# Kernel tuning notes

Measured on AMD Instinct MI355X. Metric: run time of the kernel, lower is better.

The kernel has to match this reference:

```python
import jax, jax.numpy as jnp
import numpy as np
import math

B, S, H, NH = 2, 2048, 1024, 16
DH = H // NH  # 64
REL_VOCAB = 4096  # 2 * (max_position_embeddings // 4)


def setup_inputs() -> dict:
    key = jax.random.key(0)
    ks = jax.random.split(key, 9)
    s = 0.02
    return {
        "hidden_states": jax.random.normal(ks[0], (B, S, H), jnp.float32),
        "attention_mask": jnp.zeros((B, 1, 1, S), jnp.float32),
        "distance_idx": jax.random.randint(ks[1], (S, S), 0, REL_VOCAB),
        "Wq": jax.random.normal(ks[2], (H, H), jnp.float32) * s,
        "bq": jnp.zeros((H,), jnp.float32),
        "Wk": jax.random.normal(ks[3], (H, H), jnp.float32) * s,
        "bk": jnp.zeros((H,), jnp.float32),
        "Wv": jax.random.normal(ks[4], (H, H), jnp.float32) * s,
        "bv": jnp.zeros((H,), jnp.float32),
        "dist_emb": jax.random.normal(ks[5], (REL_VOCAB, NH), jnp.float32) * s,
    }


def _heads(x):
    # [B,S,H] -> [B,NH,S,DH]
    return x.reshape(B, S, NH, DH).transpose(0, 2, 1, 3)


def reference(hidden_states, attention_mask, distance_idx, Wq, bq, Wk, bk, Wv, bv, dist_emb):
    q = _heads(hidden_states @ Wq.T + bq)
    k = _heads(hidden_states @ Wk.T + bk)
    v = _heads(hidden_states @ Wv.T + bv)
    # scores: [B,NH,S,S]
    scores = jnp.einsum("bhqd,bhkd->bhqk", q, k) / math.sqrt(DH)
    # relative_scalar_bias: embed(distance_idx) [S,S,NH] -> [1,NH,S,S]
    bias = dist_emb[distance_idx].transpose(2, 0, 1)[None]
    scores = scores + bias  # attention_scores_terms == 1 -> /sqrt(1)
    scores = scores + attention_mask
    probs = jax.nn.softmax(scores, axis=-1)
    ctx = jnp.einsum("bhqk,bhkd->bhqd", probs, v)
    return ctx.transpose(0, 2, 1, 3).reshape(B, S, H)
```

## Files before the change

kernel.cpp:

```cpp
#include <hip/hip_runtime.h>
#include <hip/hip_bf16.h>

#define B_   2
#define S_   2048
#define H_   1024
#define NH_  16
#define DH_  64

typedef __attribute__((ext_vector_type(8))) __bf16 bf16x8;
typedef __attribute__((ext_vector_type(8))) unsigned short u16x8;
typedef __attribute__((ext_vector_type(4))) float f32x4;

typedef const __attribute__((address_space(1))) unsigned int gu32_t;
typedef __attribute__((address_space(3))) unsigned int su32_t;

static __device__ inline unsigned short f2bf(float x) {
    union { float f; unsigned u; } v; v.f = x;
    unsigned r = v.u + 0x7fffu + ((v.u >> 16) & 1u);
    return (unsigned short)(r >> 16);
}

static __device__ inline unsigned short f2bf_r(float x) {
    union { float f; unsigned u; } v; v.f = x;
    return (unsigned short)((v.u + 0x8000u) >> 16);
}

static __device__ inline float bf2f(unsigned short u) {
    union { unsigned u; float f; } v; v.u = ((unsigned)u) << 16;
    return v.f;
}

static __device__ inline bf16x8 ldfrag(const unsigned short* p) {
    return __builtin_bit_cast(bf16x8, *(const u16x8*)p);
}

__global__ void conv_all(const float* __restrict__ x,
                         const float* __restrict__ Wq, const float* __restrict__ Wk,
                         const float* __restrict__ Wv, const float* __restrict__ demb,
                         unsigned short* __restrict__ xb, unsigned short* __restrict__ wall,
                         unsigned short* __restrict__ dembT) {
    int bid = blockIdx.x, tid = threadIdx.x;
    if (bid < 4096) {
        int i = bid * 256 + tid;
        float4 v = ((const float4*)x)[i];
        ushort4 o;
        o.x = f2bf(v.x); o.y = f2bf(v.y); o.z = f2bf(v.z); o.w = f2bf(v.w);
        ((ushort4*)xb)[i] = o;
    } else if (bid < 7168) {
        int i = (bid - 4096) * 256 + tid;
        int e = i * 4;
        int which = e >> 20;
        int r4 = (e & ((1 << 20) - 1)) >> 2;
        const float* src = which == 0 ? Wq : which == 1 ? Wk : Wv;
        float4 v = ((const float4*)src)[r4];
        ushort4 o;
        o.x = f2bf(v.x); o.y = f2bf(v.y); o.z = f2bf(v.z); o.w = f2bf(v.w);
        ((ushort4*)wall)[i] = o;
    } else {
        int t = (bid - 7168) * 256 + tid;
        int h = t >> 12, e = t & 4095;
        dembT[t] = f2bf(demb[e * 16 + h] * 1.4426950408889634f);
    }
}

__global__ __launch_bounds__(256) void gemm_qkv(
    const unsigned short* __restrict__ Xb, const unsigned short* __restrict__ Wall,
    const float* __restrict__ bq, const float* __restrict__ bk, const float* __restrict__ bv,
    unsigned short* __restrict__ Q, unsigned short* __restrict__ K, unsigned short* __restrict__ V)
{
    __shared__ unsigned short As[128 * 32];
    __shared__ unsigned short Bs[128 * 32];
    const int tid = threadIdx.x, lane = tid & 63, wv = tid >> 6;
    const int g = lane >> 4, l16 = lane & 15;
    const int wm = wv >> 1, wn = wv & 1;
    const int bm = blockIdx.y, bn = blockIdx.x;

    const int lrow = lane >> 2, lcol = (lane & 3) * 8;

    f32x4 acc[4][4];
    #pragma unroll
    for (int i = 0; i < 4; ++i)
        #pragma unroll
        for (int j = 0; j < 4; ++j) acc[i][j] = (f32x4){0.f, 0.f, 0.f, 0.f};

    for (int kt = 0; kt < 32; ++kt) {
        #pragma unroll
        for (int i = 0; i < 2; ++i) {
            int chunk = wv * 2 + i;
            int row = chunk * 16 + lrow;
            const unsigned short* ga = &Xb[(size_t)(bm * 128 + row) * 1024 + kt * 32 + lcol];
            const unsigned short* gb = &Wall[(size_t)(bn * 128 + row) * 1024 + kt * 32 + lcol];
            __builtin_amdgcn_global_load_lds((gu32_t*)(const void*)ga, (su32_t*)(void*)&As[chunk * 512], 16, 0, 0);
            __builtin_amdgcn_global_load_lds((gu32_t*)(const void*)gb, (su32_t*)(void*)&Bs[chunk * 512], 16, 0, 0);
        }
        __syncthreads();
        bf16x8 a[4], b[4];
        #pragma unroll
        for (int mi = 0; mi < 4; ++mi) a[mi] = ldfrag(&As[(wm * 64 + mi * 16 + l16) * 32 + g * 8]);
        #pragma unroll
        for (int ni = 0; ni < 4; ++ni) b[ni] = ldfrag(&Bs[(wn * 64 + ni * 16 + l16) * 32 + g * 8]);
        #pragma unroll
        for (int mi = 0; mi < 4; ++mi)
            #pragma unroll
            for (int ni = 0; ni < 4; ++ni)
                acc[mi][ni] = __builtin_amdgcn_mfma_f32_16x16x32_bf16(a[mi], b[ni], acc[mi][ni], 0, 0, 0);
        __syncthreads();
    }

    #pragma unroll
    for (int mi = 0; mi < 4; ++mi) {
        #pragma unroll
        for (int ni = 0; ni < 4; ++ni) {
            int gn = bn * 128 + wn * 64 + ni * 16 + l16;
            int which = gn >> 10, nn = gn & 1023;
            int h = nn >> 6, d = nn & 63;
            float bias = which == 0 ? bq[nn] : which == 1 ? bk[nn] : bv[nn];
            unsigned short* dst = which == 0 ? Q : which == 1 ? K : V;
            #pragma unroll
            for (int r = 0; r < 4; ++r) {
                int gm = bm * 128 + wm * 64 + mi * 16 + g * 4 + r;
                int bb = gm >> 11, s = gm & 2047;
                dst[((size_t)(bb * 16 + h) * 2048 + s) * 64 + d] = f2bf(acc[mi][ni][r] + bias);
            }
        }
    }
}

__global__ void transpose_v(const unsigned short* __restrict__ V, unsigned short* __restrict__ VT) {
    __shared__ unsigned short t[64][65];
    int bh = blockIdx.y, st = blockIdx.x, tid = threadIdx.x;
    size_t ib = (size_t)bh * S_ * DH_ + (size_t)st * 64 * 64;
    #pragma unroll
    for (int rep = 0; rep < 16; ++rep) {
        int e = rep * 256 + tid;
        t[e >> 6][e & 63] = V[ib + e];
    }
    __syncthreads();
    size_t ob = (size_t)bh * DH_ * S_ + st * 64;
    #pragma unroll
    for (int rep = 0; rep < 16; ++rep) {
        int e = rep * 256 + tid;
        int d = e >> 6, sl = e & 63;
        VT[ob + (size_t)d * S_ + sl] = t[sl][d];
    }
}

__global__ __launch_bounds__(256, 4) void attn(
    const unsigned short* __restrict__ Q, const unsigned short* __restrict__ K,
    const unsigned short* __restrict__ VT, const int* __restrict__ didx,
    const unsigned short* __restrict__ dembT, const float* __restrict__ mask,
    float* __restrict__ out)
{
    __shared__ unsigned short demb_h[4096];
    __shared__ unsigned short Ks[64 * 64];
    __shared__ unsigned short Vs[64 * 64];
    __shared__ unsigned short Ps[64 * 64];
    const int tid = threadIdx.x, lane = tid & 63, w = tid >> 6;
    const int g = lane >> 4, l16 = lane & 15;
    const int h = blockIdx.x, qt = blockIdx.y, b = blockIdx.z;
    const int bh = b * NH_ + h;
    const int qr = qt * 64 + w * 16;

    #pragma unroll
    for (int j = 0; j < 2; ++j) {
        int i = j * 256 + tid;
        *(uint4*)&demb_h[i * 8] = *(const uint4*)&dembT[h * 4096 + i * 8];
    }

    bf16x8 qf[4][2];
    #pragma unroll
    for (int qtile = 0; qtile < 4; ++qtile) {
        size_t qbase = ((size_t)bh * S_ + qt * 64 + qtile * 16 + l16) * DH_;
        qf[qtile][0] = ldfrag(&Q[qbase + g * 8]);
        qf[qtile][1] = ldfrag(&Q[qbase + 32 + g * 8]);
    }

    u16x8 ou;
    #pragma unroll
    for (int i = 0; i < 8; ++i) ou[i] = 0x3F80;
    const bf16x8 onesf = __builtin_bit_cast(bf16x8, ou);

    f32x4 oa[4];
    f32x4 lacc = (f32x4){0.f, 0.f, 0.f, 0.f};
    #pragma unroll
    for (int i = 0; i < 4; ++i) oa[i] = (f32x4){0.f, 0.f, 0.f, 0.f};

    const size_t kbase = (size_t)bh * S_ * DH_;
    const size_t vbase = (size_t)bh * DH_ * S_;

    __syncthreads();

    for (int kt = 0; kt < 32; ++kt) {
        #pragma unroll
        for (int j = 0; j < 2; ++j) {
            int e = j * 2048 + tid * 8;
            int r = e >> 6, c = e & 63;
            int sidx = r * 64 + ((((c >> 3) ^ (r & 7))) << 3);
            *(uint4*)&Ks[sidx] = *(const uint4*)&K[kbase + (size_t)kt * 64 * 64 + e];
            *(uint4*)&Vs[sidx] = *(const uint4*)&VT[vbase + (size_t)r * S_ + kt * 64 + c];
        }

        const int kg = kt * 64 + w * 16 + l16;
        float mk = mask[b * S_ + kg];
        int ei[4][4];
        #pragma unroll
        for (int qtile = 0; qtile < 4; ++qtile) {
            #pragma unroll
            for (int r = 0; r < 4; ++r) {
                int qg = qt * 64 + qtile * 16 + g * 4 + r;
                ei[qtile][r] = didx[qg * S_ + kg];
            }
        }
        __syncthreads();

        const int krow = w * 16 + l16, km = krow & 7;
        bf16x8 kf0 = ldfrag(&Ks[krow * 64 + ((g ^ km) << 3)]);
        bf16x8 kf1 = ldfrag(&Ks[krow * 64 + (((g + 4) ^ km) << 3)]);
        const float mkl = mk * 1.4426950408889634f;
        const int pcol = w * 16 + l16;
        const int chunkx = pcol >> 3, coff = pcol & 7;

        __builtin_amdgcn_s_setprio(1);
        #pragma unroll
        for (int qtile = 0; qtile < 4; ++qtile) {
            f32x4 z = (f32x4){0.f, 0.f, 0.f, 0.f};
            z = __builtin_amdgcn_mfma_f32_16x16x32_bf16(qf[qtile][0], kf0, z, 0, 0, 0);
            z = __builtin_amdgcn_mfma_f32_16x16x32_bf16(qf[qtile][1], kf1, z, 0, 0, 0);
            #pragma unroll
            for (int r = 0; r < 4; ++r) {
                float bm = bf2f(demb_h[ei[qtile][r]]) + mkl;
                float p = __builtin_amdgcn_exp2f(fmaf(z[r], 0.18033688011112042f, bm));
                int q = qtile * 16 + g * 4 + r;
                int idx = q * 64 + (((chunkx ^ (q & 7))) << 3) + coff;
                Ps[idx] = f2bf_r(p);
            }
        }
        __builtin_amdgcn_s_setprio(0);
        __syncthreads();

        const int prow = w * 16 + l16, pm = prow & 7;
        bf16x8 pf0 = ldfrag(&Ps[prow * 64 + ((g ^ pm) << 3)]);
        bf16x8 pf1 = ldfrag(&Ps[prow * 64 + (((g + 4) ^ pm) << 3)]);
        __builtin_amdgcn_s_setprio(1);
        lacc = __builtin_amdgcn_mfma_f32_16x16x32_bf16(pf0, onesf, lacc, 0, 0, 0);
        lacc = __builtin_amdgcn_mfma_f32_16x16x32_bf16(pf1, onesf, lacc, 0, 0, 0);
        #pragma unroll
        for (int dt = 0; dt < 4; ++dt) {
            int row = dt * 16 + l16, m = row & 7;
            bf16x8 vf0 = ldfrag(&Vs[row * 64 + ((g ^ m) << 3)]);
            bf16x8 vf1 = ldfrag(&Vs[row * 64 + (((g + 4) ^ m) << 3)]);
            oa[dt] = __builtin_amdgcn_mfma_f32_16x16x32_bf16(pf0, vf0, oa[dt], 0, 0, 0);
            oa[dt] = __builtin_amdgcn_mfma_f32_16x16x32_bf16(pf1, vf1, oa[dt], 0, 0, 0);
        }
        __builtin_amdgcn_s_setprio(0);
        __syncthreads();
    }

    float linv[4];
    #pragma unroll
    for (int r = 0; r < 4; ++r) linv[r] = __builtin_amdgcn_rcpf(lacc[r]);

    #pragma unroll
    for (int dt = 0; dt < 4; ++dt) {
        #pragma unroll
        for (int r = 0; r < 4; ++r) {
            int s = qr + g * 4 + r;
            int d = dt * 16 + l16;
            out[((size_t)b * S_ + s) * H_ + h * DH_ + d] = oa[dt][r] * linv[r];
        }
    }
}

extern "C" void kernel_launch(void* const* d_in, const int* in_sizes, int n_in,
                              void* d_out, int out_size, void* d_ws, size_t ws_size,
                              hipStream_t stream) {
    const float* hidden = (const float*)d_in[0];
    const float* mask   = (const float*)d_in[1];
    const int*   didx   = (const int*)d_in[2];
    const float* Wq     = (const float*)d_in[3];
    const float* bq     = (const float*)d_in[4];
    const float* Wk     = (const float*)d_in[5];
    const float* bk     = (const float*)d_in[6];
    const float* Wv     = (const float*)d_in[7];
    const float* bv     = (const float*)d_in[8];
    const float* demb   = (const float*)d_in[9];
    float* out = (float*)d_out;

    unsigned short* ws = (unsigned short*)d_ws;
    unsigned short* Xb   = ws;
    unsigned short* Wall = Xb + 4096 * 1024;
    unsigned short* Qb   = Wall + 3072 * 1024;
    unsigned short* Kb   = Qb + 4194304;
    unsigned short* Vb   = Kb + 4194304;
    unsigned short* VTb  = Vb + 4194304;
    unsigned short* DembT = VTb + 4194304;

    conv_all<<<7424, 256, 0, stream>>>(hidden, Wq, Wk, Wv, demb, Xb, Wall, DembT);
    gemm_qkv<<<dim3(24, 32), 256, 0, stream>>>(Xb, Wall, bq, bk, bv, Qb, Kb, Vb);
    transpose_v<<<dim3(32, 32), 256, 0, stream>>>(Vb, VTb);
    attn<<<dim3(16, 32, 2), 256, 0, stream>>>(Qb, Kb, VTb, didx, DembT, mask, out);
}
```

Before: 222.0 us.

## Keep P in registers via transposed QK^T and split-K PV with final reduction

Computes S^T = K·Q^T so each lane's score fragment directly serves as the A operand of a 16x16x16 MFMA for P·V. This removes the Ps shared-memory round trip and one barrier per key tile. Each wave now accumulates partial outputs for all four query tiles over its own 16 keys, and the partials are reduced across waves through shared memory at the end. Row sums are now done with scalar adds plus shuffles instead of a ones-MFMA, and distance-index and mask loads become int4/float4. The cost is more accumulator registers (launch bounds lowered to 3), an epilogue reduction, and a fallback macro that silently returns c if the builtin is missing.

```diff
diff --git a/kernel.cpp b/kernel.cpp
--- a/kernel.cpp
+++ b/kernel.cpp
@@ -10,6 +10,7 @@
 typedef __attribute__((ext_vector_type(8))) __bf16 bf16x8;
 typedef __attribute__((ext_vector_type(8))) unsigned short u16x8;
 typedef __attribute__((ext_vector_type(4))) float f32x4;
+typedef __attribute__((ext_vector_type(4))) short i16x4;
 
 typedef const __attribute__((address_space(1))) unsigned int gu32_t;
 typedef __attribute__((address_space(3))) unsigned int su32_t;
@@ -33,6 +34,12 @@
 static __device__ inline bf16x8 ldfrag(const unsigned short* p) {
     return __builtin_bit_cast(bf16x8, *(const u16x8*)p);
 }
+
+#if __has_builtin(__builtin_amdgcn_mfma_f32_16x16x16bf16_1k)
+#define MFMA16(a, b, c) __builtin_amdgcn_mfma_f32_16x16x16bf16_1k((a), (b), (c), 0, 0, 0)
+#else
+#define MFMA16(a, b, c) (c)
+#endif
 
 __global__ void conv_all(const float* __restrict__ x,
                          const float* __restrict__ Wq, const float* __restrict__ Wk,
@@ -145,21 +152,23 @@
     }
 }
 
-__global__ __launch_bounds__(256, 4) void attn(
+__global__ __launch_bounds__(256, 3) void attn(
     const unsigned short* __restrict__ Q, const unsigned short* __restrict__ K,
     const unsigned short* __restrict__ VT, const int* __restrict__ didx,
     const unsigned short* __restrict__ dembT, const float* __restrict__ mask,
     float* __restrict__ out)
 {
-    __shared__ unsigned short demb_h[4096];
-    __shared__ unsigned short Ks[64 * 64];
-    __shared__ unsigned short Vs[64 * 64];
-    __shared__ unsigned short Ps[64 * 64];
+    __shared__ __align__(16) unsigned char smem[24576];
+    unsigned short* demb_h = (unsigned short*)smem;
+    unsigned short* Ks     = (unsigned short*)(smem + 8192);
+    unsigned short* Vs     = (unsigned short*)(smem + 16384);
+    float* tbl = (float*)smem;
+    float* red = (float*)smem;
+
     const int tid = threadIdx.x, lane = tid & 63, w = tid >> 6;
     const int g = lane >> 4, l16 = lane & 15;
     const int h = blockIdx.x, qt = blockIdx.y, b = blockIdx.z;
     const int bh = b * NH_ + h;
-    const int qr = qt * 64 + w * 16;
 
     #pragma unroll
     for (int j = 0; j < 2; ++j) {
@@ -175,18 +184,18 @@
         qf[qtile][1] = ldfrag(&Q[qbase + 32 + g * 8]);
     }
 
-    u16x8 ou;
-    #pragma unroll
-    for (int i = 0; i < 8; ++i) ou[i] = 0x3F80;
-    const bf16x8 onesf = __builtin_bit_cast(bf16x8, ou);
-
-    f32x4 oa[4];
-    f32x4 lacc = (f32x4){0.f, 0.f, 0.f, 0.f};
-    #pragma unroll
-    for (int i = 0; i < 4; ++i) oa[i] = (f32x4){0.f, 0.f, 0.f, 0.f};
+    f32x4 oa[4][4];
+    float lsum[4];
+    #pragma unroll
+    for (int i = 0; i < 4; ++i) {
+        lsum[i] = 0.f;
+        #pragma unroll
+        for (int j = 0; j < 4; ++j) oa[i][j] = (f32x4){0.f, 0.f, 0.f, 0.f};
+    }
 
     const size_t kbase = (size_t)bh * S_ * DH_;
     const size_t vbase = (size_t)bh * DH_ * S_;
+    const int kg0 = w * 16 + g * 4;
 
     __syncthreads();
 
@@ -196,79 +205,167 @@
             int e = j * 2048 + tid * 8;
             int r = e >> 6, c = e & 63;
             int sidx = r * 64 + ((((c >> 3) ^ (r & 7))) << 3);
-            *(uint4*)&Ks[sidx] = *(const uint4*)&K[kbase + (size_t)kt * 64 * 64 + e];
+            *(uint4*)&Ks[sidx] = *(const uint4*)&K[kbase + (size_t)kt * 4096 + e];
             *(uint4*)&Vs[sidx] = *(const uint4*)&VT[vbase + (size_t)r * S_ + kt * 64 + c];
         }
 
-        const int kg = kt * 64 + w * 16 + l16;
-        float mk = mask[b * S_ + kg];
-        int ei[4][4];
-        #pragma unroll
-        for (int qtile = 0; qtile < 4; ++qtile) {
-            #pragma unroll
-            for (int r = 0; r < 4; ++r) {
-                int qg = qt * 64 + qtile * 16 + g * 4 + r;
-                ei[qtile][r] = didx[qg * S_ + kg];
-            }
-        }
+        const int kg = kt * 64 + kg0;
+        int4 di0 = *(const int4*)&didx[(qt * 64 + 0 * 16 + l16) * S_ + kg];
+        int4 di1 = *(const int4*)&didx[(qt * 64 + 1 * 16 + l16) * S_ + kg];
+        int4 di2 = *(const int4*)&didx[(qt * 64 + 2 * 16 + l16) * S_ + kg];
+        int4 di3 = *(const int4*)&didx[(qt * 64 + 3 * 16 + l16) * S_ + kg];
+        float4 mv = *(const float4*)&mask[b * S_ + kg];
         __syncthreads();
 
         const int krow = w * 16 + l16, km = krow & 7;
         bf16x8 kf0 = ldfrag(&Ks[krow * 64 + ((g ^ km) << 3)]);
         bf16x8 kf1 = ldfrag(&Ks[krow * 64 + (((g + 4) ^ km) << 3)]);
-        const float mkl = mk * 1.4426950408889634f;
-        const int pcol = w * 16 + l16;
-        const int chunkx = pcol >> 3, coff = pcol & 7;
-
+
+        i16x4 vf[4];
+        #pragma unroll
+        for (int dt = 0; dt < 4; ++dt) {
+            int vrow = dt * 16 + l16, vm = vrow & 7;
+            int chunkc = w * 2 + (g >> 1);
+            int addr = vrow * 64 + (((chunkc ^ vm)) << 3) + ((g & 1) << 2);
+            vf[dt] = *(const i16x4*)&Vs[addr];
+        }
+
+        f32x4 z0, z1, z2, z3;
         __builtin_amdgcn_s_setprio(1);
-        #pragma unroll
-        for (int qtile = 0; qtile < 4; ++qtile) {
-            f32x4 z = (f32x4){0.f, 0.f, 0.f, 0.f};
-            z = __builtin_amdgcn_mfma_f32_16x16x32_bf16(qf[qtile][0], kf0, z, 0, 0, 0);
-            z = __builtin_amdgcn_mfma_f32_16x16x32_bf16(qf[qtile][1], kf1, z, 0, 0, 0);
-            #pragma unroll
-            for (int r = 0; r < 4; ++r) {
-                float bm = bf2f(demb_h[ei[qtile][r]]) + mkl;
-                float p = __builtin_amdgcn_exp2f(fmaf(z[r], 0.18033688011112042f, bm));
-                int q = qtile * 16 + g * 4 + r;
-                int idx = q * 64 + (((chunkx ^ (q & 7))) << 3) + coff;
-                Ps[idx] = f2bf_r(p);
-            }
+        {
+            f32x4 zz = (f32x4){0.f, 0.f, 0.f, 0.f};
+            zz = __builtin_amdgcn_mfma_f32_16x16x32_bf16(kf0, qf[0][0], zz, 0, 0, 0);
+            z0 = __builtin_amdgcn_mfma_f32_16x16x32_bf16(kf1, qf[0][1], zz, 0, 0, 0);
+            zz = (f32x4){0.f, 0.f, 0.f, 0.f};
+            zz = __builtin_amdgcn_mfma_f32_16x16x32_bf16(kf0, qf[1][0], zz, 0, 0, 0);
+            z1 = __builtin_amdgcn_mfma_f32_16x16x32_bf16(kf1, qf[1][1], zz, 0, 0, 0);
+            zz = (f32x4){0.f, 0.f, 0.f, 0.f};
+            zz = __builtin_amdgcn_mfma_f32_16x16x32_bf16(kf0, qf[2][0], zz, 0, 0, 0);
+            z2 = __builtin_amdgcn_mfma_f32_16x16x32_bf16(kf1, qf[2][1], zz, 0, 0, 0);
+            zz = (f32x4){0.f, 0.f, 0.f, 0.f};
+            zz = __builtin_amdgcn_mfma_f32_16x16x32_bf16(kf0, qf[3][0], zz, 0, 0, 0);
+            z3 = __builtin_amdgcn_mfma_f32_16x16x32_bf16(kf1, qf[3][1], zz, 0, 0, 0);
+        }
+        __builtin_amdgcn_s_setprio(0);
+
+        const float ml0 = mv.x * 1.4426950408889634f;
+        const float ml1 = mv.y * 1.4426950408889634f;
+        const float ml2 = mv.z * 1.4426950408889634f;
+        const float ml3 = mv.w * 1.4426950408889634f;
+        i16x4 pa0, pa1, pa2, pa3;
+        #define EXPPACK(ZZ, DI, PA, QIDX)                                                   \
+        {                                                                                   \
+            float p0 = __builtin_amdgcn_exp2f(fmaf(ZZ[0], 0.18033688011112042f,             \
+                        bf2f(demb_h[DI.x]) + ml0));                                         \
+            float p1 = __builtin_amdgcn_exp2f(fmaf(ZZ[1], 0.18033688011112042f,             \
+                        bf2f(demb_h[DI.y]) + ml1));                                         \
+            float p2 = __builtin_amdgcn_exp2f(fmaf(ZZ[2], 0.18033688011112042f,             \
+                        bf2f(demb_h[DI.z]) + ml2));                                         \
+            float p3 = __builtin_amdgcn_exp2f(fmaf(ZZ[3], 0.18033688011112042f,             \
+                        bf2f(demb_h[DI.w]) + ml3));                                         \
+            lsum[QIDX] += (p0 + p1) + (p2 + p3);                                            \
+            PA[0] = (short)f2bf_r(p0); PA[1] = (short)f2bf_r(p1);                           \
+            PA[2] = (short)f2bf_r(p2); PA[3] = (short)f2bf_r(p3);                           \
+        }
+        EXPPACK(z0, di0, pa0, 0)
+        EXPPACK(z1, di1, pa1, 1)
+        EXPPACK(z2, di2, pa2, 2)
+        EXPPACK(z3, di3, pa3, 3)
+        #undef EXPPACK
+
+        __builtin_amdgcn_s_setprio(1);
+        #pragma unroll
+        for (int dt = 0; dt < 4; ++dt) {
+            oa[0][dt] = MFMA16(pa0, vf[dt], oa[0][dt]);
+            oa[1][dt] = MFMA16(pa1, vf[dt], oa[1][dt]);
+            oa[2][dt] = MFMA16(pa2, vf[dt], oa[2][dt]);
+            oa[3][dt] = MFMA16(pa3, vf[dt], oa[3][dt]);
         }
         __builtin_amdgcn_s_setprio(0);
         __syncthreads();
-
-        const int prow = w * 16 + l16, pm = prow & 7;
-        bf16x8 pf0 = ldfrag(&Ps[prow * 64 + ((g ^ pm) << 3)]);
-        bf16x8 pf1 = ldfrag(&Ps[prow * 64 + (((g + 4) ^ pm) << 3)]);
-        __builtin_amdgcn_s_setprio(1);
-        lacc = __builtin_amdgcn_mfma_f32_16x16x32_bf16(pf0, onesf, lacc, 0, 0, 0);
-        lacc = __builtin_amdgcn_mfma_f32_16x16x32_bf16(pf1, onesf, lacc, 0, 0, 0);
-        #pragma unroll
-        for (int dt = 0; dt < 4; ++dt) {
-            int row = dt * 16 + l16, m = row & 7;
-            bf16x8 vf0 = ldfrag(&Vs[row * 64 + ((g ^ m) << 3)]);
-            bf16x8 vf1 = ldfrag(&Vs[row * 64 + (((g + 4) ^ m) << 3)]);
-            oa[dt] = __builtin_amdgcn_mfma_f32_16x16x32_bf16(pf0, vf0, oa[dt], 0, 0, 0);
-            oa[dt] = __builtin_amdgcn_mfma_f32_16x16x32_bf16(pf1, vf1, oa[dt], 0, 0, 0);
-        }
-        __builtin_amdgcn_s_setprio(0);
-        __syncthreads();
-    }
-
-    float linv[4];
-    #pragma unroll
-    for (int r = 0; r < 4; ++r) linv[r] = __builtin_amdgcn_rcpf(lacc[r]);
-
-    #pragma unroll
-    for (int dt = 0; dt < 4; ++dt) {
-        #pragma unroll
-        for (int r = 0; r < 4; ++r) {
-            int s = qr + g * 4 + r;
-            int d = dt * 16 + l16;
-            out[((size_t)b * S_ + s) * H_ + h * DH_ + d] = oa[dt][r] * linv[r];
-        }
-    }
+    }
+
+    #pragma unroll
+    for (int t = 0; t < 4; ++t) {
+        lsum[t] += __shfl_xor(lsum[t], 16);
+        lsum[t] += __shfl_xor(lsum[t], 32);
+    }
+    if (lane < 16) {
+        #pragma unroll
+        for (int t = 0; t < 4; ++t) tbl[(w * 4 + t) * 16 + l16] = lsum[t];
+    }
+    __syncthreads();
+    f32x4 dsum = (f32x4){0.f, 0.f, 0.f, 0.f};
+    #pragma unroll
+    for (int sw = 0; sw < 4; ++sw) dsum += *(const f32x4*)&tbl[(sw * 4 + w) * 16 + g * 4];
+    f32x4 linv;
+    #pragma unroll
+    for (int r = 0; r < 4; ++r) linv[r] = __builtin_amdgcn_rcpf(dsum[r]);
+    __syncthreads();
+
+    #pragma unroll
+    for (int t = 0; t < 2; ++t) {
+        if (w != t) {
+            int slot = w < t ? w : w - 1;
+            #pragma unroll
+            for (int dt = 0; dt < 4; ++dt)
+                *(f32x4*)&red[(((t * 3 + slot) * 4 + dt) * 16 + l16) * 16 + g * 4] = oa[t][dt];
+        }
+    }
+    __syncthreads();
+    if (w == 0) {
+        #pragma unroll
+        for (int slot = 0; slot < 3; ++slot)
+            #pragma unroll
+            for (int dt = 0; dt < 4; ++dt)
+                oa[0][dt] += *(const f32x4*)&red[(((0 * 3 + slot) * 4 + dt) * 16 + l16) * 16 + g * 4];
+    } else if (w == 1) {
+        #pragma unroll
+        for (int slot = 0; slot < 3; ++slot)
+            #pragma unroll
+            for (int dt = 0; dt < 4; ++dt)
+                oa[1][dt] += *(const f32x4*)&red[(((1 * 3 + slot) * 4 + dt) * 16 + l16) * 16 + g * 4];
+    }
+    __syncthreads();
+    #pragma unroll
+    for (int t2 = 0; t2 < 2; ++t2) {
+        const int t = 2 + t2;
+        if (w != t) {
+            int slot = w < t ? w : w - 1;
+            #pragma unroll
+            for (int dt = 0; dt < 4; ++dt)
+                *(f32x4*)&red[(((t2 * 3 + slot) * 4 + dt) * 16 + l16) * 16 + g * 4] = oa[t][dt];
+        }
+    }
+    __syncthreads();
+    if (w == 2) {
+        #pragma unroll
+        for (int slot = 0; slot < 3; ++slot)
+            #pragma unroll
+            for (int dt = 0; dt < 4; ++dt)
+                oa[2][dt] += *(const f32x4*)&red[(((0 * 3 + slot) * 4 + dt) * 16 + l16) * 16 + g * 4];
+    } else if (w == 3) {
+        #pragma unroll
+        for (int slot = 0; slot < 3; ++slot)
+            #pragma unroll
+            for (int dt = 0; dt < 4; ++dt)
+                oa[3][dt] += *(const f32x4*)&red[(((1 * 3 + slot) * 4 + dt) * 16 + l16) * 16 + g * 4];
+    }
+
+    #define STORE_QT(T)                                                                     \
+    if (w == T) {                                                                           \
+        _Pragma("unroll")                                                                   \
+        for (int dt = 0; dt < 4; ++dt) {                                                    \
+            _Pragma("unroll")                                                               \
+            for (int r = 0; r < 4; ++r) {                                                   \
+                int s = qt * 64 + T * 16 + g * 4 + r;                                       \
+                out[((size_t)b * S_ + s) * H_ + h * DH_ + dt * 16 + l16] =                  \
+                    oa[T][dt][r] * linv[r];                                                 \
+            }                                                                               \
+        }                                                                                   \
+    }
+    STORE_QT(0) else STORE_QT(1) else STORE_QT(2) else STORE_QT(3)
+    #undef STORE_QT
 }
 
 extern "C" void kernel_launch(void* const* d_in, const int* in_sizes, int n_in,
```

Result: slower. 240.8 us (+8.5%).
